# Kernel optimization log

Measured on AMD Instinct MI355X. Metric: run time of the kernel, lower is better.

## Reference

```python
import jax, jax.numpy as jnp
import numpy as np

N_NODES = 50000
N_EDGES = 800000
N_REL = 8
OUT_CH = 64      # latent dim of z
HID = 128        # hidden_channels
IN_CH = 128      # reconstructed feature dim
NEG_SLOPE = 0.2


def rgat_conv(x, src, dst, edge_type, weight, q, k, bias, num_nodes):
    """PyG RGATConv, heads=1, dim=1, additive-self-attention, across-relation.
    x: [N, in]; weight: [R, in, out]; q,k: [out, 1]; bias: [out]."""
    # per-relation transform of all nodes, then per-edge gather (same math as
    # per-edge bmm with weight[edge_type], avoids [E, in, out] intermediate)
    x_all = jnp.einsum('ni,rio->nro', x, weight)          # [N, R, out]
    x_j = x_all[src, edge_type]                            # [E, out]
    x_i = x_all[dst, edge_type]                            # [E, out]
    alpha = (x_i @ q + x_j @ k)[:, 0]                      # [E]
    alpha = jax.nn.leaky_relu(alpha, NEG_SLOPE)
    # scatter-softmax over destination neighborhoods
    m = jax.ops.segment_max(alpha, dst, num_segments=num_nodes)
    m = jnp.where(jnp.isfinite(m), m, 0.0)                 # empty segments -> 0
    ex = jnp.exp(alpha - m[dst])
    denom = jax.ops.segment_sum(ex, dst, num_segments=num_nodes)
    a = ex / (denom[dst] + 1e-16)                          # [E]
    out = jax.ops.segment_sum(a[:, None] * x_j, dst, num_segments=num_nodes)
    return out + bias


def setup_inputs() -> dict:
    key = jax.random.key(0)
    ks = jax.random.split(key, 12)
    z = jax.random.normal(ks[0], (N_NODES, OUT_CH), dtype=jnp.float32)
    edge_index = jax.random.randint(ks[1], (2, N_EDGES), 0, N_NODES, dtype=jnp.int32)
    edge_type = jax.random.randint(ks[2], (N_EDGES,), 0, N_REL, dtype=jnp.int32)

    def glorot(k_, shape):
        fan = shape[-2] + shape[-1]
        return jax.random.normal(k_, shape, dtype=jnp.float32) * jnp.sqrt(2.0 / fan)

    return {
        'z': z,
        'lin_w': glorot(ks[3], (HID, OUT_CH)),
        'lin_b': jnp.zeros((HID,), dtype=jnp.float32),
        'w1': glorot(ks[4], (N_REL, HID, HID)),
        'q1': glorot(ks[5], (HID, 1)),
        'k1': glorot(ks[6], (HID, 1)),
        'b1': jnp.zeros((HID,), dtype=jnp.float32),
        'w2': glorot(ks[7], (N_REL, HID, IN_CH)),
        'q2': glorot(ks[8], (IN_CH, 1)),
        'k2': glorot(ks[9], (IN_CH, 1)),
        'b2': jnp.zeros((IN_CH,), dtype=jnp.float32),
        'edge_index': edge_index,
        'edge_type': edge_type,
    }


def reference(z, lin_w, lin_b, w1, q1, k1, b1, w2, q2, k2, b2, edge_index, edge_type):
    num_nodes = z.shape[0]
    src, dst = edge_index[0], edge_index[1]
    h = z @ lin_w.T + lin_b                                 # nn.Linear
    h = jax.nn.relu(rgat_conv(h, src, dst, edge_type, w1, q1, k1, b1, num_nodes))
    # dropout is identity in eval mode
    recon_x = rgat_conv(h, src, dst, edge_type, w2, q2, k2, b2, num_nodes)
    return recon_x
```

## Files before the change

### kernel.cpp

```cpp
#include <hip/hip_runtime.h>
#include <hip/hip_bf16.h>
#include <cstdint>
#include <cstddef>

#define N_NODES 50000
#define N_EDGES 800000
#define NSEG    (N_NODES * 8)

using frag_t = __attribute__((ext_vector_type(8))) short;
using f32x4  = __attribute__((ext_vector_type(4))) float;

typedef const __attribute__((address_space(1))) void* gptr_t;
typedef __attribute__((address_space(3))) void* lptr_t;

__device__ __forceinline__ short f2bf(float x) {
    __hip_bfloat16 h = __float2bfloat16(x);
    return *reinterpret_cast<short*>(&h);
}
__device__ __forceinline__ float bf2f(unsigned int u) {
    union { unsigned int i; float f; } v;
    v.i = u << 16;
    return v.f;
}
__device__ __forceinline__ float bf2f_hi(unsigned int u) {
    union { unsigned int i; float f; } v;
    v.i = u & 0xFFFF0000u;
    return v.f;
}
__device__ __forceinline__ unsigned int packbf2(float lo, float hi) {
    unsigned int a = (unsigned short)f2bf(lo);
    unsigned int b = (unsigned short)f2bf(hi);
    return a | (b << 16);
}


__global__ void hist_kernel(const int* __restrict__ dst, const int* __restrict__ et,
                            int* __restrict__ deg8, int E) {
    int e = blockIdx.x * 256 + threadIdx.x;
    if (e < E) atomicAdd(&deg8[dst[e] * 8 + et[e]], 1);
}

__global__ __launch_bounds__(256) void scan_part(const int* __restrict__ deg8,
                                                 int* __restrict__ part, int M) {
    __shared__ int red[256];
    int t = threadIdx.x;
    int idx = blockIdx.x * 1024 + t * 4;
    int s = 0;
    if (idx + 3 < M) {
        int4 d = *(const int4*)(deg8 + idx);
        s = d.x + d.y + d.z + d.w;
    } else {
        for (int c = 0; c < 4; c++) if (idx + c < M) s += deg8[idx + c];
    }
    red[t] = s;
    __syncthreads();
    #pragma unroll
    for (int off = 128; off; off >>= 1) {
        if (t < off) red[t] += red[t + off];
        __syncthreads();
    }
    if (t == 0) part[blockIdx.x] = red[0];
}

__global__ __launch_bounds__(512) void scan_mid(int* __restrict__ part, int nparts,
                                                int* __restrict__ rowp, int M) {
    __shared__ int buf[512];
    int t = threadIdx.x;
    int own = (t < nparts) ? part[t] : 0;
    buf[t] = own;
    __syncthreads();
    for (int off = 1; off < 512; off <<= 1) {
        int v = buf[t];
        int u = (t >= off) ? buf[t - off] : 0;
        __syncthreads();
        buf[t] = v + u;
        __syncthreads();
    }
    if (t < nparts) part[t] = buf[t] - own;
    if (t == 511) rowp[M] = buf[511];
}

__global__ __launch_bounds__(256) void scan_fix(const int* __restrict__ deg8,
                                                const int* __restrict__ part,
                                                int* __restrict__ rowp,
                                                int* __restrict__ cursor, int M) {
    __shared__ int wsum[4];
    int t = threadIdx.x, lane = t & 63, w = t >> 6;
    int idx = blockIdx.x * 1024 + t * 4;
    int v0 = 0, v1 = 0, v2 = 0, v3 = 0;
    if (idx + 3 < M) {
        int4 d = *(const int4*)(deg8 + idx);
        v0 = d.x; v1 = d.y; v2 = d.z; v3 = d.w;
    } else {
        if (idx     < M) v0 = deg8[idx];
        if (idx + 1 < M) v1 = deg8[idx + 1];
        if (idx + 2 < M) v2 = deg8[idx + 2];
        if (idx + 3 < M) v3 = deg8[idx + 3];
    }
    int tsum = v0 + v1 + v2 + v3;
    int sc = tsum;
    #pragma unroll
    for (int off = 1; off < 64; off <<= 1) {
        int u = __shfl_up(sc, off, 64);
        if (lane >= off) sc += u;
    }
    if (lane == 63) wsum[w] = sc;
    __syncthreads();
    int woff = 0;
    for (int i = 0; i < w; i++) woff += wsum[i];
    int excl = part[blockIdx.x] + woff + sc - tsum;
    if (idx     < M) { rowp[idx]     = excl; cursor[idx]     = excl; } excl += v0;
    if (idx + 1 < M) { rowp[idx + 1] = excl; cursor[idx + 1] = excl; } excl += v1;
    if (idx + 2 < M) { rowp[idx + 2] = excl; cursor[idx + 2] = excl; } excl += v2;
    if (idx + 3 < M) { rowp[idx + 3] = excl; cursor[idx + 3] = excl; }
}

__global__ void fill_kernel(const int* __restrict__ src, const int* __restrict__ dst,
                            const int* __restrict__ et, int* __restrict__ cursor,
                            int* __restrict__ sorted, int E) {
    int e = blockIdx.x * 256 + threadIdx.x;
    if (e < E) {
        int pos = atomicAdd(&cursor[dst[e] * 8 + et[e]], 1);
        sorted[pos] = src[e] | (et[e] << 16);
    }
}


__global__ __launch_bounds__(256) void gemm_lin(const float* __restrict__ A,
                                                const float* __restrict__ B,
                                                const float* __restrict__ bias,
                                                unsigned short* __restrict__ hb, int N) {
    const int Kdim = 64;
    __shared__ float As[32][64];
    __shared__ float Bs[32][128];
    int t = threadIdx.x;
    int n0 = blockIdx.x * 64;
    int rg = t >> 4, cg = t & 15;
    int an = t >> 2, ak = (t & 3) * 8;
    float acc[4][8] = {};

    for (int k0 = 0; k0 < Kdim; k0 += 32) {
        int gn = n0 + an;
        if (gn < N) {
            const float* ap = A + (size_t)gn * Kdim + k0 + ak;
            float4 v0 = *(const float4*)ap;
            float4 v1 = *(const float4*)(ap + 4);
            As[ak + 0][an] = v0.x; As[ak + 1][an] = v0.y;
            As[ak + 2][an] = v0.z; As[ak + 3][an] = v0.w;
            As[ak + 4][an] = v1.x; As[ak + 5][an] = v1.y;
            As[ak + 6][an] = v1.z; As[ak + 7][an] = v1.w;
        } else {
            #pragma unroll
            for (int c = 0; c < 8; c++) As[ak + c][an] = 0.f;
        }
        {
            int o = t >> 1, kh = (t & 1) * 16;
            const float* bp = B + (size_t)o * Kdim + k0 + kh;
            #pragma unroll
            for (int j = 0; j < 4; j++) {
                float4 v = ((const float4*)bp)[j];
                Bs[kh + j * 4 + 0][o] = v.x;
                Bs[kh + j * 4 + 1][o] = v.y;
                Bs[kh + j * 4 + 2][o] = v.z;
                Bs[kh + j * 4 + 3][o] = v.w;
            }
        }
        __syncthreads();
        #pragma unroll
        for (int k = 0; k < 32; k++) {
            float a[4], b[8];
            *(float4*)&a[0] = *(const float4*)&As[k][rg * 4];
            *(float4*)&b[0] = *(const float4*)&Bs[k][cg * 8];
            *(float4*)&b[4] = *(const float4*)&Bs[k][cg * 8 + 4];
            #pragma unroll
            for (int i = 0; i < 4; i++)
                #pragma unroll
                for (int j = 0; j < 8; j++)
                    acc[i][j] = fmaf(a[i], b[j], acc[i][j]);
        }
        __syncthreads();
    }
    #pragma unroll
    for (int i = 0; i < 4; i++) {
        int gn = n0 + rg * 4 + i;
        if (gn < N) {
            unsigned short us[8];
            #pragma unroll
            for (int j = 0; j < 8; j++)
                us[j] = (unsigned short)f2bf(acc[i][j] + bias[cg * 8 + j]);
            *(int4*)(hb + (size_t)gn * 128 + cg * 8) = *(int4*)&us[0];
        }
    }
}


__global__ void wprep2_kernel(const float* __restrict__ W1, const float* __restrict__ q1v,
                              const float* __restrict__ k1v,
                              const float* __restrict__ W2, const float* __restrict__ q2v,
                              const float* __restrict__ k2v,
                              short* __restrict__ Bf1, short* __restrict__ Bf2,
                              float* __restrict__ wq1, float* __restrict__ wk1,
                              float* __restrict__ wq2, float* __restrict__ wk2) {
    int g0 = blockIdx.x * 256 + threadIdx.x;
    int layer = (g0 >= 133120) ? 1 : 0;
    int g = g0 - layer * 133120;
    const float* W  = layer ? W2  : W1;
    const float* qv = layer ? q2v : q1v;
    const float* kv = layer ? k2v : k1v;
    short* Bf = layer ? Bf2 : Bf1;
    float* wq = layer ? wq2 : wq1;
    float* wk = layer ? wk2 : wk1;

    if (g < 131072) {
        int kk = g >> 7, o = g & 127;
        float v = W[(size_t)kk * 128 + o];
        Bf[(((size_t)(kk >> 3) * 128) + o) * 8 + (kk & 7)] = f2bf(v);
        return;
    }
    int h = g - 131072;
    if (h < 2048) {
        int which = h >> 10;
        int r = (h >> 7) & 7;
        int i = h & 127;
        const float* vec = which ? kv : qv;
        const float* wrow = W + ((size_t)r * 128 + i) * 128;
        float acc = 0.f;
        #pragma unroll 4
        for (int o = 0; o < 128; o++) acc = fmaf(wrow[o], vec[o], acc);
        (which ? wk : wq)[r * 128 + i] = acc;
    }
}


__global__ __launch_bounds__(256) void qk_table_kernel(const unsigned short* __restrict__ xb,
                                                       const float* __restrict__ wq,
                                                       const float* __restrict__ wk,
                                                       float* __restrict__ Q,
                                                       float* __restrict__ K, int N) {
    int n = blockIdx.x * 256 + threadIdx.x;
    if (n >= N) return;
    const uint2* row = (const uint2*)(xb + (size_t)n * 128);
    float aq[8] = {}, ak[8] = {};
    for (int i = 0; i < 32; i++) {
        uint2 d = row[i];
        float x0 = bf2f(d.x & 0xFFFFu);
        float x1 = bf2f(d.x >> 16);
        float x2 = bf2f(d.y & 0xFFFFu);
        float x3 = bf2f(d.y >> 16);
        int c = i * 4;
        #pragma unroll
        for (int r = 0; r < 8; r++) {
            const float* wqr = wq + r * 128 + c;
            const float* wkr = wk + r * 128 + c;
            aq[r] = fmaf(x0, wqr[0], fmaf(x1, wqr[1], fmaf(x2, wqr[2], fmaf(x3, wqr[3], aq[r]))));
            ak[r] = fmaf(x0, wkr[0], fmaf(x1, wkr[1], fmaf(x2, wkr[2], fmaf(x3, wkr[3], ak[r]))));
        }
    }
    float4* qp = (float4*)(Q + (size_t)n * 8);
    qp[0] = *(float4*)&aq[0];
    qp[1] = *(float4*)&aq[4];
    float4* kp = (float4*)(K + (size_t)n * 8);
    kp[0] = *(float4*)&ak[0];
    kp[1] = *(float4*)&ak[4];
}


__global__ __launch_bounds__(512, 8) void fused_agg_gemm(
        const unsigned short* __restrict__ hb,
        const float* __restrict__ Q,
        const float* __restrict__ Kt,
        const int* __restrict__ rowp8,
        const int* __restrict__ sorted,
        const short* __restrict__ Bf,
        const float* __restrict__ bias,
        float* __restrict__ Cout,
        unsigned short* __restrict__ hbout,
        int N, int relu) {
    __shared__ short s_tile[16 * 1024];
    __shared__ uint2 stash[8][64];
    __shared__ int wcnt;
    unsigned int* sdw = (unsigned int*)s_tile;
    const char* hbB = (const char*)hb;

    int t = threadIdx.x;
    int w = t >> 6, lane = t & 63;
    int lhi = lane >> 4, llo = lane & 15;
    unsigned int lv4 = (unsigned int)lane * 4u;
    int n0 = blockIdx.x * 16;

    if (t == 0) wcnt = 0;
    __syncthreads();

    for (;;) {
        int row;
        if (lane == 0) row = atomicAdd(&wcnt, 1);
        row = __shfl(row, 0, 64);
        if (row >= 16) break;
        int n = n0 + row;
        float2 acc = {0.f, 0.f};
        int rcur = 0;
        auto flushw = [&](unsigned int val) {
            int kb = rcur * 16 + (lane >> 2);
            sdw[kb * 64 + ((row ^ (kb & 15)) * 4) + (lane & 3)] = val;
        };
        if (n >= N) {
            while (rcur < 8) { flushw(0u); rcur++; }
            continue;
        }
        int beg = rowp8[n * 8];
        int end = rowp8[n * 8 + 8];
        int deg = end - beg;
        if (deg == 0) {
            while (rcur < 8) { flushw(0u); rcur++; }
            continue;
        }

        if (deg <= 64) {
            int pk = 0;
            float a = -INFINITY;
            if (lane < deg) {
                pk = sorted[beg + lane];
                int srcn = pk & 0xFFFF, etj = pk >> 16;
                a = Q[(size_t)n * 8 + etj] + Kt[(size_t)srcn * 8 + etj];
                a = (a > 0.f) ? a : 0.2f * a;
            }
            float m = a;
            #pragma unroll
            for (int off = 32; off; off >>= 1) m = fmaxf(m, __shfl_xor(m, off, 64));
            float e = (lane < deg) ? __expf(a - m) : 0.f;
            float sum = e;
            #pragma unroll
            for (int off = 32; off; off >>= 1) sum += __shfl_xor(sum, off, 64);
            float wgt = e / (sum + 1e-16f);
            stash[w][lane] = make_uint2((unsigned int)(pk & 0xFFFF) << 8,
                                        (__float_as_uint(wgt) & ~7u) | (unsigned int)(pk >> 16));

            int j = 0;
            for (; j + 8 <= deg; j += 8) {
                uint2 ee[8]; unsigned int dd[8];
                #pragma unroll
                for (int i = 0; i < 8; i++) ee[i] = stash[w][j + i];
                #pragma unroll
                for (int i = 0; i < 8; i++)
                    dd[i] = *(const unsigned int*)(hbB + (ee[i].x | lv4));
                #pragma unroll
                for (int i = 0; i < 8; i++) {
                    int e0 = (int)(ee[i].y & 7u);
                    float w0 = __uint_as_float(ee[i].y);
                    while (rcur < e0) { flushw(packbf2(acc.x, acc.y)); acc.x = acc.y = 0.f; rcur++; }
                    acc.x = fmaf(w0, bf2f(dd[i]),    acc.x);
                    acc.y = fmaf(w0, bf2f_hi(dd[i]), acc.y);
                }
            }
            for (; j < deg; j++) {
                uint2 e1 = stash[w][j];
                unsigned int d0 = *(const unsigned int*)(hbB + (e1.x | lv4));
                int e0 = (int)(e1.y & 7u);
                float w0 = __uint_as_float(e1.y);
                while (rcur < e0) { flushw(packbf2(acc.x, acc.y)); acc.x = acc.y = 0.f; rcur++; }
                acc.x = fmaf(w0, bf2f(d0),    acc.x);
                acc.y = fmaf(w0, bf2f_hi(d0), acc.y);
            }
            while (rcur < 8) { flushw(packbf2(acc.x, acc.y)); acc.x = acc.y = 0.f; rcur++; }
        } else {
            auto logit = [&](int j) -> float {
                int pk2 = sorted[beg + j];
                int srcn = pk2 & 0xFFFF, etj = pk2 >> 16;
                float aa = Q[(size_t)n * 8 + etj] + Kt[(size_t)srcn * 8 + etj];
                return (aa > 0.f) ? aa : 0.2f * aa;
            };
            float m = -INFINITY;
            for (int j = lane; j < deg; j += 64) m = fmaxf(m, logit(j));
            #pragma unroll
            for (int off = 32; off; off >>= 1) m = fmaxf(m, __shfl_xor(m, off, 64));
            float sum = 0.f;
            for (int j = lane; j < deg; j += 64) sum += __expf(logit(j) - m);
            #pragma unroll
            for (int off = 32; off; off >>= 1) sum += __shfl_xor(sum, off, 64);
            float inv = 1.f / (sum + 1e-16f);

            for (int j0 = 0; j0 < deg; j0 += 64) {
                int cnt = min(64, deg - j0);
                if (lane < cnt) {
                    int pk = sorted[beg + j0 + lane];
                    int srcn = pk & 0xFFFF, etj = pk >> 16;
                    float aa = Q[(size_t)n * 8 + etj] + Kt[(size_t)srcn * 8 + etj];
                    aa = (aa > 0.f) ? aa : 0.2f * aa;
                    float wgt = __expf(aa - m) * inv;
                    stash[w][lane] = make_uint2((unsigned int)srcn << 8,
                                                (__float_as_uint(wgt) & ~7u) | (unsigned int)etj);
                }
                for (int j = 0; j < cnt; j++) {
                    uint2 e1 = stash[w][j];
                    unsigned int d0 = *(const unsigned int*)(hbB + (e1.x | lv4));
                    int e0 = (int)(e1.y & 7u);
                    float w0 = __uint_as_float(e1.y);
                    while (rcur < e0) { flushw(packbf2(acc.x, acc.y)); acc.x = acc.y = 0.f; rcur++; }
                    acc.x = fmaf(w0, bf2f(d0),    acc.x);
                    acc.y = fmaf(w0, bf2f_hi(d0), acc.y);
                }
            }
            while (rcur < 8) { flushw(packbf2(acc.x, acc.y)); acc.x = acc.y = 0.f; rcur++; }
        }
    }
    __syncthreads();

    int ctb = w;
    f32x4 acc0 = {};
    const char* BfB = (const char*)Bf;
    #pragma unroll 4
    for (int kq = 0; kq < 32; kq++) {
        int kb = kq * 4 + lhi;
        int d = kb * 64 + ((llo ^ (kb & 15)) * 4);
        frag_t a  = *(const frag_t*)(&sdw[d]);
        frag_t b0 = *(const frag_t*)(BfB + ((size_t)kb * 128 + ctb * 16 + llo) * 16);
        acc0 = __builtin_amdgcn_mfma_f32_16x16x32_bf16(a, b0, acc0, 0, 0, 0);
    }

    {
        int col = ctb * 16 + llo;
        float bv = bias[col];
        #pragma unroll
        for (int rg = 0; rg < 4; rg++) {
            int rown = n0 + lhi * 4 + rg;
            if (rown < N) {
                float v = acc0[rg] + bv;
                if (relu) v = fmaxf(v, 0.f);
                if (Cout)  Cout[(size_t)rown * 128 + col] = v;
                if (hbout) hbout[(size_t)rown * 128 + col] = (unsigned short)f2bf(v);
            }
        }
    }
}


extern "C" void kernel_launch(void* const* d_in, const int* in_sizes, int n_in,
                              void* d_out, int out_size, void* d_ws, size_t ws_size,
                              hipStream_t stream) {
    const float* z     = (const float*)d_in[0];
    const float* lin_w = (const float*)d_in[1];
    const float* lin_b = (const float*)d_in[2];
    const float* w1    = (const float*)d_in[3];
    const float* q1    = (const float*)d_in[4];
    const float* k1    = (const float*)d_in[5];
    const float* b1    = (const float*)d_in[6];
    const float* w2    = (const float*)d_in[7];
    const float* q2    = (const float*)d_in[8];
    const float* k2    = (const float*)d_in[9];
    const float* b2    = (const float*)d_in[10];
    const int*   ei    = (const int*)d_in[11];
    const int*   et    = (const int*)d_in[12];
    float* out = (float*)d_out;

    char* ws = (char*)d_ws;
    size_t off = 0;
    auto alloc = [&](size_t bytes) -> void* {
        void* p = ws + off;
        off += (bytes + 255) & ~(size_t)255;
        return p;
    };
    unsigned short* hb  = (unsigned short*)alloc((size_t)N_NODES * 128 * 2);
    unsigned short* hb2 = (unsigned short*)alloc((size_t)N_NODES * 128 * 2);
    float* Q     = (float*)alloc((size_t)N_NODES * 8 * 4);
    float* K     = (float*)alloc((size_t)N_NODES * 8 * 4);
    int* sorted  = (int*)alloc((size_t)N_EDGES * 4);
    int* deg8    = (int*)alloc((size_t)NSEG * 4);
    int* rowp8   = (int*)alloc((size_t)(NSEG + 1) * 4);
    int* cursor8 = (int*)alloc((size_t)NSEG * 4);
    int* part    = (int*)alloc(1024 * 4);
    float* wq1   = (float*)alloc(8 * 128 * 4);
    float* wk1   = (float*)alloc(8 * 128 * 4);
    float* wq2   = (float*)alloc(8 * 128 * 4);
    float* wk2   = (float*)alloc(8 * 128 * 4);
    short* Bf1   = (short*)alloc((size_t)1024 * 128 * 2);
    short* Bf2   = (short*)alloc((size_t)1024 * 128 * 2);

    const int* src = ei;
    const int* dst = ei + N_EDGES;

    const int M = NSEG;
    const int nparts = (M + 1023) / 1024;

    hipMemsetAsync(deg8, 0, (size_t)M * 4, stream);
    hist_kernel<<<(N_EDGES + 255) / 256, 256, 0, stream>>>(dst, et, deg8, N_EDGES);
    scan_part<<<nparts, 256, 0, stream>>>(deg8, part, M);
    scan_mid<<<1, 512, 0, stream>>>(part, nparts, rowp8, M);
    scan_fix<<<nparts, 256, 0, stream>>>(deg8, part, rowp8, cursor8, M);
    fill_kernel<<<(N_EDGES + 255) / 256, 256, 0, stream>>>(src, dst, et, cursor8, sorted, N_EDGES);

    gemm_lin<<<(N_NODES + 63) / 64, 256, 0, stream>>>(z, lin_w, lin_b, hb, N_NODES);

    wprep2_kernel<<<(2 * 133120 + 255) / 256, 256, 0, stream>>>(
        w1, q1, k1, w2, q2, k2, Bf1, Bf2, wq1, wk1, wq2, wk2);

    int fgrid = (N_NODES + 15) / 16;
    int qgrid = (N_NODES + 255) / 256;

    qk_table_kernel<<<qgrid, 256, 0, stream>>>(hb, wq1, wk1, Q, K, N_NODES);
    fused_agg_gemm<<<fgrid, 512, 0, stream>>>(hb, Q, K, rowp8, sorted, Bf1, b1,
                                              (float*)nullptr, hb2, N_NODES, 1);

    qk_table_kernel<<<qgrid, 256, 0, stream>>>(hb2, wq2, wk2, Q, K, N_NODES);
    fused_agg_gemm<<<fgrid, 512, 0, stream>>>(hb2, Q, K, rowp8, sorted, Bf2, b2,
                                              out, (unsigned short*)nullptr, N_NODES, 0);
}
```

Baseline: 370.3 us.

## Fuse per-node Q/K attention tables into the producing GEMM epilogues

Removes both standalone qk_table kernels. The linear-layer GEMM and the first aggregation+GEMM kernel now compute the next layer's per-relation Q/K projections in their epilogues, reading the freshly produced bf16 rows from shared memory. This avoids re-reading the hidden feature matrices from global memory and saves two launches. In exchange it adds extra barriers and epilogue work to the fused kernels, and it needs separate Q/K buffers for layer two so the second layer does not overwrite tables the first layer is still reading.

```diff
diff --git a/kernel.cpp b/kernel.cpp
--- a/kernel.cpp
+++ b/kernel.cpp
@@ -126,13 +126,18 @@
 }
 
 
-__global__ __launch_bounds__(256) void gemm_lin(const float* __restrict__ A,
-                                                const float* __restrict__ B,
-                                                const float* __restrict__ bias,
-                                                unsigned short* __restrict__ hb, int N) {
+__global__ __launch_bounds__(256) void gemm_lin_qk(const float* __restrict__ A,
+                                                   const float* __restrict__ B,
+                                                   const float* __restrict__ bias,
+                                                   const float* __restrict__ wq,
+                                                   const float* __restrict__ wk,
+                                                   unsigned short* __restrict__ hb,
+                                                   float* __restrict__ Q,
+                                                   float* __restrict__ Kt, int N) {
     const int Kdim = 64;
-    __shared__ float As[32][64];
-    __shared__ float Bs[32][128];
+    __shared__ float smem[32 * 64 + 32 * 128];
+    float (*As)[64]  = (float (*)[64])smem;
+    float (*Bs)[128] = (float (*)[128])(smem + 32 * 64);
     int t = threadIdx.x;
     int n0 = blockIdx.x * 64;
     int rg = t >> 4, cg = t & 15;
@@ -180,15 +185,54 @@
         }
         __syncthreads();
     }
+
+    unsigned short* hlds = (unsigned short*)smem;
     #pragma unroll
     for (int i = 0; i < 4; i++) {
         int gn = n0 + rg * 4 + i;
-        if (gn < N) {
-            unsigned short us[8];
-            #pragma unroll
-            for (int j = 0; j < 8; j++)
-                us[j] = (unsigned short)f2bf(acc[i][j] + bias[cg * 8 + j]);
+        unsigned short us[8];
+        #pragma unroll
+        for (int j = 0; j < 8; j++)
+            us[j] = (unsigned short)f2bf(acc[i][j] + bias[cg * 8 + j]);
+        if (gn < N)
             *(int4*)(hb + (size_t)gn * 128 + cg * 8) = *(int4*)&us[0];
+        *(int4*)(hlds + (size_t)(rg * 4 + i) * 128 + cg * 8) = *(int4*)&us[0];
+    }
+    __syncthreads();
+
+    {
+        int n = t >> 2, qq = t & 3;
+        int gn = n0 + n;
+        float aq[8] = {}, akk[8] = {};
+        const uint2* rowq = (const uint2*)(hlds + (size_t)n * 128 + qq * 32);
+        #pragma unroll
+        for (int i = 0; i < 8; i++) {
+            uint2 d = rowq[i];
+            float x0 = bf2f(d.x & 0xFFFFu);
+            float x1 = bf2f(d.x >> 16);
+            float x2 = bf2f(d.y & 0xFFFFu);
+            float x3 = bf2f(d.y >> 16);
+            int c = qq * 32 + i * 4;
+            #pragma unroll
+            for (int r = 0; r < 8; r++) {
+                const float* wqr = wq + r * 128 + c;
+                const float* wkr = wk + r * 128 + c;
+                aq[r]  = fmaf(x0, wqr[0], fmaf(x1, wqr[1], fmaf(x2, wqr[2], fmaf(x3, wqr[3], aq[r]))));
+                akk[r] = fmaf(x0, wkr[0], fmaf(x1, wkr[1], fmaf(x2, wkr[2], fmaf(x3, wkr[3], akk[r]))));
+            }
+        }
+        #pragma unroll
+        for (int r = 0; r < 8; r++) {
+            aq[r]  += __shfl_xor(aq[r], 1, 64);  aq[r]  += __shfl_xor(aq[r], 2, 64);
+            akk[r] += __shfl_xor(akk[r], 1, 64); akk[r] += __shfl_xor(akk[r], 2, 64);
+        }
+        if (qq == 0 && gn < N) {
+            float4* qp = (float4*)(Q + (size_t)gn * 8);
+            qp[0] = *(float4*)&aq[0];
+            qp[1] = *(float4*)&aq[4];
+            float4* kp = (float4*)(Kt + (size_t)gn * 8);
+            kp[0] = *(float4*)&akk[0];
+            kp[1] = *(float4*)&akk[4];
         }
     }
 }
@@ -232,39 +276,6 @@
 }
 
 
-__global__ __launch_bounds__(256) void qk_table_kernel(const unsigned short* __restrict__ xb,
-                                                       const float* __restrict__ wq,
-                                                       const float* __restrict__ wk,
-                                                       float* __restrict__ Q,
-                                                       float* __restrict__ K, int N) {
-    int n = blockIdx.x * 256 + threadIdx.x;
-    if (n >= N) return;
-    const uint2* row = (const uint2*)(xb + (size_t)n * 128);
-    float aq[8] = {}, ak[8] = {};
-    for (int i = 0; i < 32; i++) {
-        uint2 d = row[i];
-        float x0 = bf2f(d.x & 0xFFFFu);
-        float x1 = bf2f(d.x >> 16);
-        float x2 = bf2f(d.y & 0xFFFFu);
-        float x3 = bf2f(d.y >> 16);
-        int c = i * 4;
-        #pragma unroll
-        for (int r = 0; r < 8; r++) {
-            const float* wqr = wq + r * 128 + c;
-            const float* wkr = wk + r * 128 + c;
-            aq[r] = fmaf(x0, wqr[0], fmaf(x1, wqr[1], fmaf(x2, wqr[2], fmaf(x3, wqr[3], aq[r]))));
-            ak[r] = fmaf(x0, wkr[0], fmaf(x1, wkr[1], fmaf(x2, wkr[2], fmaf(x3, wkr[3], ak[r]))));
-        }
-    }
-    float4* qp = (float4*)(Q + (size_t)n * 8);
-    qp[0] = *(float4*)&aq[0];
-    qp[1] = *(float4*)&aq[4];
-    float4* kp = (float4*)(K + (size_t)n * 8);
-    kp[0] = *(float4*)&ak[0];
-    kp[1] = *(float4*)&ak[4];
-}
-
-
 __global__ __launch_bounds__(512, 8) void fused_agg_gemm(
         const unsigned short* __restrict__ hb,
         const float* __restrict__ Q,
@@ -273,6 +284,10 @@
         const int* __restrict__ sorted,
         const short* __restrict__ Bf,
         const float* __restrict__ bias,
+        const float* __restrict__ wqn,
+        const float* __restrict__ wkn,
+        float* __restrict__ Qout,
+        float* __restrict__ Kout,
         float* __restrict__ Cout,
         unsigned short* __restrict__ hbout,
         int N, int relu) {
@@ -417,17 +432,50 @@
         acc0 = __builtin_amdgcn_mfma_f32_16x16x32_bf16(a, b0, acc0, 0, 0, 0);
     }
 
+    unsigned short us2[4];
+    int col = ctb * 16 + llo;
     {
-        int col = ctb * 16 + llo;
         float bv = bias[col];
         #pragma unroll
         for (int rg = 0; rg < 4; rg++) {
+            float v = acc0[rg] + bv;
+            if (relu) v = fmaxf(v, 0.f);
+            us2[rg] = (unsigned short)f2bf(v);
             int rown = n0 + lhi * 4 + rg;
             if (rown < N) {
-                float v = acc0[rg] + bv;
-                if (relu) v = fmaxf(v, 0.f);
                 if (Cout)  Cout[(size_t)rown * 128 + col] = v;
-                if (hbout) hbout[(size_t)rown * 128 + col] = (unsigned short)f2bf(v);
+                if (hbout) hbout[(size_t)rown * 128 + col] = us2[rg];
+            }
+        }
+    }
+
+    if (Qout) {
+        __syncthreads();
+        unsigned short* qlds = (unsigned short*)s_tile;
+        #pragma unroll
+        for (int rg = 0; rg < 4; rg++)
+            qlds[(size_t)(lhi * 4 + rg) * 128 + col] = us2[rg];
+        __syncthreads();
+        if (t < 256) {
+            int n = t >> 4;
+            int rr = (t >> 1) & 7;
+            int which = t & 1;
+            int gn = n0 + n;
+            if (gn < N) {
+                const float* wv = which ? wkn : wqn;
+                const uint2* rowq = (const uint2*)(qlds + (size_t)n * 128);
+                float acc = 0.f;
+                #pragma unroll 8
+                for (int i = 0; i < 32; i++) {
+                    uint2 d = rowq[i];
+                    float x0 = bf2f(d.x & 0xFFFFu);
+                    float x1 = bf2f(d.x >> 16);
+                    float x2 = bf2f(d.y & 0xFFFFu);
+                    float x3 = bf2f(d.y >> 16);
+                    const float* wv4 = wv + rr * 128 + i * 4;
+                    acc = fmaf(x0, wv4[0], fmaf(x1, wv4[1], fmaf(x2, wv4[2], fmaf(x3, wv4[3], acc))));
+                }
+                (which ? Kout : Qout)[(size_t)gn * 8 + rr] = acc;
             }
         }
     }
@@ -463,6 +511,8 @@
     unsigned short* hb2 = (unsigned short*)alloc((size_t)N_NODES * 128 * 2);
     float* Q     = (float*)alloc((size_t)N_NODES * 8 * 4);
     float* K     = (float*)alloc((size_t)N_NODES * 8 * 4);
+    float* Qb    = (float*)alloc((size_t)N_NODES * 8 * 4);
+    float* Kb    = (float*)alloc((size_t)N_NODES * 8 * 4);
     int* sorted  = (int*)alloc((size_t)N_EDGES * 4);
     int* deg8    = (int*)alloc((size_t)NSEG * 4);
     int* rowp8   = (int*)alloc((size_t)(NSEG + 1) * 4);
@@ -488,19 +538,20 @@
     scan_fix<<<nparts, 256, 0, stream>>>(deg8, part, rowp8, cursor8, M);
     fill_kernel<<<(N_EDGES + 255) / 256, 256, 0, stream>>>(src, dst, et, cursor8, sorted, N_EDGES);
 
-    gemm_lin<<<(N_NODES + 63) / 64, 256, 0, stream>>>(z, lin_w, lin_b, hb, N_NODES);
-
     wprep2_kernel<<<(2 * 133120 + 255) / 256, 256, 0, stream>>>(
         w1, q1, k1, w2, q2, k2, Bf1, Bf2, wq1, wk1, wq2, wk2);
 
+    gemm_lin_qk<<<(N_NODES + 63) / 64, 256, 0, stream>>>(z, lin_w, lin_b, wq1, wk1,
+                                                         hb, Q, K, N_NODES);
+
     int fgrid = (N_NODES + 15) / 16;
-    int qgrid = (N_NODES + 255) / 256;
-
-    qk_table_kernel<<<qgrid, 256, 0, stream>>>(hb, wq1, wk1, Q, K, N_NODES);
+
     fused_agg_gemm<<<fgrid, 512, 0, stream>>>(hb, Q, K, rowp8, sorted, Bf1, b1,
+                                              wq2, wk2, Qb, Kb,
                                               (float*)nullptr, hb2, N_NODES, 1);
 
-    qk_table_kernel<<<qgrid, 256, 0, stream>>>(hb2, wq2, wk2, Q, K, N_NODES);
-    fused_agg_gemm<<<fgrid, 512, 0, stream>>>(hb2, Q, K, rowp8, sorted, Bf2, b2,
+    fused_agg_gemm<<<fgrid, 512, 0, stream>>>(hb2, Qb, Kb, rowp8, sorted, Bf2, b2,
+                                              (const float*)nullptr, (const float*)nullptr,
+                                              (float*)nullptr, (float*)nullptr,
                                               out, (unsigned short*)nullptr, N_NODES, 0);
 }
```

After: 428.1 us. 1.16x slower.

## Merge independent prep kernels into block-partitioned mega-kernels to cut launches

Applied to the files above, without the earlier changes.

Combines the edge histogram, weight preparation and the input linear GEMM into one launch, with block ranges selecting each role. Also merges the CSR fill pass with the layer-1 Q/K table computation, since they do not depend on each other. The goal is fewer kernel launches and letting independent work overlap on the GPU. In exchange, all blocks now carry the GEMM's shared-memory footprint and register pressure, which may lower occupancy for the lightweight histogram blocks.

```diff
diff --git a/kernel.cpp b/kernel.cpp
--- a/kernel.cpp
+++ b/kernel.cpp
@@ -6,6 +6,10 @@
 #define N_NODES 50000
 #define N_EDGES 800000
 #define NSEG    (N_NODES * 8)
+#define HIST_BLKS 3125
+#define WPREP_BLKS 1040
+#define GLIN_BLKS 782
+#define QK_BLKS 196
 
 using frag_t = __attribute__((ext_vector_type(8))) short;
 using f32x4  = __attribute__((ext_vector_type(4))) float;
@@ -34,11 +38,125 @@
 }
 
 
-__global__ void hist_kernel(const int* __restrict__ dst, const int* __restrict__ et,
-                            int* __restrict__ deg8, int E) {
-    int e = blockIdx.x * 256 + threadIdx.x;
-    if (e < E) atomicAdd(&deg8[dst[e] * 8 + et[e]], 1);
-}
+__global__ __launch_bounds__(256) void prep_mega(
+        const int* __restrict__ dst, const int* __restrict__ et,
+        int* __restrict__ deg8,
+        const float* __restrict__ W1, const float* __restrict__ q1v,
+        const float* __restrict__ k1v,
+        const float* __restrict__ W2, const float* __restrict__ q2v,
+        const float* __restrict__ k2v,
+        short* __restrict__ Bf1, short* __restrict__ Bf2,
+        float* __restrict__ wq1, float* __restrict__ wk1,
+        float* __restrict__ wq2, float* __restrict__ wk2,
+        const float* __restrict__ z, const float* __restrict__ lin_w,
+        const float* __restrict__ lin_b,
+        unsigned short* __restrict__ hb) {
+    __shared__ float smem[32 * 64 + 32 * 128];
+    int b = blockIdx.x, t = threadIdx.x;
+
+    if (b < HIST_BLKS) {
+        int e = b * 256 + t;
+        if (e < N_EDGES) atomicAdd(&deg8[dst[e] * 8 + et[e]], 1);
+        return;
+    }
+    b -= HIST_BLKS;
+
+    if (b < WPREP_BLKS) {
+        int g0 = b * 256 + t;
+        int layer = (g0 >= 133120) ? 1 : 0;
+        int g = g0 - layer * 133120;
+        const float* W  = layer ? W2  : W1;
+        const float* qv = layer ? q2v : q1v;
+        const float* kv = layer ? k2v : k1v;
+        short* Bf = layer ? Bf2 : Bf1;
+        float* wq = layer ? wq2 : wq1;
+        float* wk = layer ? wk2 : wk1;
+        if (g < 131072) {
+            int kk = g >> 7, o = g & 127;
+            float v = W[(size_t)kk * 128 + o];
+            Bf[(((size_t)(kk >> 3) * 128) + o) * 8 + (kk & 7)] = f2bf(v);
+        } else {
+            int h = g - 131072;
+            if (h < 2048) {
+                int which = h >> 10;
+                int r = (h >> 7) & 7;
+                int i = h & 127;
+                const float* vec = which ? kv : qv;
+                const float* wrow = W + ((size_t)r * 128 + i) * 128;
+                float acc = 0.f;
+                #pragma unroll 4
+                for (int o = 0; o < 128; o++) acc = fmaf(wrow[o], vec[o], acc);
+                (which ? wk : wq)[r * 128 + i] = acc;
+            }
+        }
+        return;
+    }
+    b -= WPREP_BLKS;
+
+    {
+        float (*As)[64]  = (float (*)[64])smem;
+        float (*Bs)[128] = (float (*)[128])(smem + 32 * 64);
+        const int Kdim = 64;
+        int n0 = b * 64;
+        int rg = t >> 4, cg = t & 15;
+        int an = t >> 2, ak = (t & 3) * 8;
+        float acc[4][8] = {};
+
+        for (int k0 = 0; k0 < Kdim; k0 += 32) {
+            int gn = n0 + an;
+            if (gn < N_NODES) {
+                const float* ap = z + (size_t)gn * Kdim + k0 + ak;
+                float4 v0 = *(const float4*)ap;
+                float4 v1 = *(const float4*)(ap + 4);
+                As[ak + 0][an] = v0.x; As[ak + 1][an] = v0.y;
+                As[ak + 2][an] = v0.z; As[ak + 3][an] = v0.w;
+                As[ak + 4][an] = v1.x; As[ak + 5][an] = v1.y;
+                As[ak + 6][an] = v1.z; As[ak + 7][an] = v1.w;
+            } else {
+                #pragma unroll
+                for (int c = 0; c < 8; c++) As[ak + c][an] = 0.f;
+            }
+            {
+                int o = t >> 1, kh = (t & 1) * 16;
+                const float* bp = lin_w + (size_t)o * Kdim + k0 + kh;
+                #pragma unroll
+                for (int j = 0; j < 4; j++) {
+                    float4 v = ((const float4*)bp)[j];
+                    Bs[kh + j * 4 + 0][o] = v.x;
+                    Bs[kh + j * 4 + 1][o] = v.y;
+                    Bs[kh + j * 4 + 2][o] = v.z;
+                    Bs[kh + j * 4 + 3][o] = v.w;
+                }
+            }
+            __syncthreads();
+            #pragma unroll
+            for (int k = 0; k < 32; k++) {
+                float a[4], bb[8];
+                *(float4*)&a[0] = *(const float4*)&As[k][rg * 4];
+                *(float4*)&bb[0] = *(const float4*)&Bs[k][cg * 8];
+                *(float4*)&bb[4] = *(const float4*)&Bs[k][cg * 8 + 4];
+                #pragma unroll
+                for (int i = 0; i < 4; i++)
+                    #pragma unroll
+                    for (int j = 0; j < 8; j++)
+                        acc[i][j] = fmaf(a[i], bb[j], acc[i][j]);
+            }
+            __syncthreads();
+        }
+        #pragma unroll
+        for (int i = 0; i < 4; i++) {
+            int gn = n0 + rg * 4 + i;
+            if (gn < N_NODES) {
+                unsigned short us[8];
+                #pragma unroll
+                for (int j = 0; j < 8; j++)
+                    us[j] = (unsigned short)f2bf(acc[i][j] + lin_b[cg * 8 + j]);
+                *(int4*)(hb + (size_t)gn * 128 + cg * 8) = *(int4*)&us[0];
+            }
+        }
+    }
+}
+
 
 __global__ __launch_bounds__(256) void scan_part(const int* __restrict__ deg8,
                                                  int* __restrict__ part, int M) {
@@ -115,120 +233,51 @@
     if (idx + 3 < M) { rowp[idx + 3] = excl; cursor[idx + 3] = excl; }
 }
 
-__global__ void fill_kernel(const int* __restrict__ src, const int* __restrict__ dst,
-                            const int* __restrict__ et, int* __restrict__ cursor,
-                            int* __restrict__ sorted, int E) {
-    int e = blockIdx.x * 256 + threadIdx.x;
-    if (e < E) {
-        int pos = atomicAdd(&cursor[dst[e] * 8 + et[e]], 1);
-        sorted[pos] = src[e] | (et[e] << 16);
-    }
-}
-
-
-__global__ __launch_bounds__(256) void gemm_lin(const float* __restrict__ A,
-                                                const float* __restrict__ B,
-                                                const float* __restrict__ bias,
-                                                unsigned short* __restrict__ hb, int N) {
-    const int Kdim = 64;
-    __shared__ float As[32][64];
-    __shared__ float Bs[32][128];
-    int t = threadIdx.x;
-    int n0 = blockIdx.x * 64;
-    int rg = t >> 4, cg = t & 15;
-    int an = t >> 2, ak = (t & 3) * 8;
-    float acc[4][8] = {};
-
-    for (int k0 = 0; k0 < Kdim; k0 += 32) {
-        int gn = n0 + an;
-        if (gn < N) {
-            const float* ap = A + (size_t)gn * Kdim + k0 + ak;
-            float4 v0 = *(const float4*)ap;
-            float4 v1 = *(const float4*)(ap + 4);
-            As[ak + 0][an] = v0.x; As[ak + 1][an] = v0.y;
-            As[ak + 2][an] = v0.z; As[ak + 3][an] = v0.w;
-            As[ak + 4][an] = v1.x; As[ak + 5][an] = v1.y;
-            As[ak + 6][an] = v1.z; As[ak + 7][an] = v1.w;
-        } else {
-            #pragma unroll
-            for (int c = 0; c < 8; c++) As[ak + c][an] = 0.f;
-        }
-        {
-            int o = t >> 1, kh = (t & 1) * 16;
-            const float* bp = B + (size_t)o * Kdim + k0 + kh;
-            #pragma unroll
-            for (int j = 0; j < 4; j++) {
-                float4 v = ((const float4*)bp)[j];
-                Bs[kh + j * 4 + 0][o] = v.x;
-                Bs[kh + j * 4 + 1][o] = v.y;
-                Bs[kh + j * 4 + 2][o] = v.z;
-                Bs[kh + j * 4 + 3][o] = v.w;
-            }
-        }
-        __syncthreads();
+
+__global__ __launch_bounds__(256) void fill_qk(
+        const int* __restrict__ src, const int* __restrict__ dst,
+        const int* __restrict__ et, int* __restrict__ cursor,
+        int* __restrict__ sorted,
+        const unsigned short* __restrict__ xb,
+        const float* __restrict__ wq, const float* __restrict__ wk,
+        float* __restrict__ Q, float* __restrict__ K) {
+    int b = blockIdx.x, t = threadIdx.x;
+
+    if (b < HIST_BLKS) {
+        int e = b * 256 + t;
+        if (e < N_EDGES) {
+            int pos = atomicAdd(&cursor[dst[e] * 8 + et[e]], 1);
+            sorted[pos] = src[e] | (et[e] << 16);
+        }
+        return;
+    }
+    b -= HIST_BLKS;
+
+    int n = b * 256 + t;
+    if (n >= N_NODES) return;
+    const uint2* row = (const uint2*)(xb + (size_t)n * 128);
+    float aq[8] = {}, ak[8] = {};
+    for (int i = 0; i < 32; i++) {
+        uint2 d = row[i];
+        float x0 = bf2f(d.x & 0xFFFFu);
+        float x1 = bf2f(d.x >> 16);
+        float x2 = bf2f(d.y & 0xFFFFu);
+        float x3 = bf2f(d.y >> 16);
+        int c = i * 4;
         #pragma unroll
-        for (int k = 0; k < 32; k++) {
-            float a[4], b[8];
-            *(float4*)&a[0] = *(const float4*)&As[k][rg * 4];
-            *(float4*)&b[0] = *(const float4*)&Bs[k][cg * 8];
-            *(float4*)&b[4] = *(const float4*)&Bs[k][cg * 8 + 4];
-            #pragma unroll
-            for (int i = 0; i < 4; i++)
-                #pragma unroll
-                for (int j = 0; j < 8; j++)
-                    acc[i][j] = fmaf(a[i], b[j], acc[i][j]);
-        }
-        __syncthreads();
-    }
-    #pragma unroll
-    for (int i = 0; i < 4; i++) {
-        int gn = n0 + rg * 4 + i;
-        if (gn < N) {
-            unsigned short us[8];
-            #pragma unroll
-            for (int j = 0; j < 8; j++)
-                us[j] = (unsigned short)f2bf(acc[i][j] + bias[cg * 8 + j]);
-            *(int4*)(hb + (size_t)gn * 128 + cg * 8) = *(int4*)&us[0];
-        }
-    }
-}
-
-
-__global__ void wprep2_kernel(const float* __restrict__ W1, const float* __restrict__ q1v,
-                              const float* __restrict__ k1v,
-                              const float* __restrict__ W2, const float* __restrict__ q2v,
-                              const float* __restrict__ k2v,
-                              short* __restrict__ Bf1, short* __restrict__ Bf2,
-                              float* __restrict__ wq1, float* __restrict__ wk1,
-                              float* __restrict__ wq2, float* __restrict__ wk2) {
-    int g0 = blockIdx.x * 256 + threadIdx.x;
-    int layer = (g0 >= 133120) ? 1 : 0;
-    int g = g0 - layer * 133120;
-    const float* W  = layer ? W2  : W1;
-    const float* qv = layer ? q2v : q1v;
-    const float* kv = layer ? k2v : k1v;
-    short* Bf = layer ? Bf2 : Bf1;
-    float* wq = layer ? wq2 : wq1;
-    float* wk = layer ? wk2 : wk1;
-
-    if (g < 131072) {
-        int kk = g >> 7, o = g & 127;
-        float v = W[(size_t)kk * 128 + o];
-        Bf[(((size_t)(kk >> 3) * 128) + o) * 8 + (kk & 7)] = f2bf(v);
-        return;
-    }
-    int h = g - 131072;
-    if (h < 2048) {
-        int which = h >> 10;
-        int r = (h >> 7) & 7;
-        int i = h & 127;
-        const float* vec = which ? kv : qv;
-        const float* wrow = W + ((size_t)r * 128 + i) * 128;
-        float acc = 0.f;
-        #pragma unroll 4
-        for (int o = 0; o < 128; o++) acc = fmaf(wrow[o], vec[o], acc);
-        (which ? wk : wq)[r * 128 + i] = acc;
-    }
+        for (int r = 0; r < 8; r++) {
+            const float* wqr = wq + r * 128 + c;
+            const float* wkr = wk + r * 128 + c;
+            aq[r] = fmaf(x0, wqr[0], fmaf(x1, wqr[1], fmaf(x2, wqr[2], fmaf(x3, wqr[3], aq[r]))));
+            ak[r] = fmaf(x0, wkr[0], fmaf(x1, wkr[1], fmaf(x2, wkr[2], fmaf(x3, wkr[3], ak[r]))));
+        }
+    }
+    float4* qp = (float4*)(Q + (size_t)n * 8);
+    qp[0] = *(float4*)&aq[0];
+    qp[1] = *(float4*)&aq[4];
+    float4* kp = (float4*)(K + (size_t)n * 8);
+    kp[0] = *(float4*)&ak[0];
+    kp[1] = *(float4*)&ak[4];
 }
 
 
@@ -482,25 +531,27 @@
     const int nparts = (M + 1023) / 1024;
 
     hipMemsetAsync(deg8, 0, (size_t)M * 4, stream);
-    hist_kernel<<<(N_EDGES + 255) / 256, 256, 0, stream>>>(dst, et, deg8, N_EDGES);
+
+    prep_mega<<<HIST_BLKS + WPREP_BLKS + GLIN_BLKS, 256, 0, stream>>>(
+        dst, et, deg8,
+        w1, q1, k1, w2, q2, k2, Bf1, Bf2, wq1, wk1, wq2, wk2,
+        z, lin_w, lin_b, hb);
+
     scan_part<<<nparts, 256, 0, stream>>>(deg8, part, M);
     scan_mid<<<1, 512, 0, stream>>>(part, nparts, rowp8, M);
     scan_fix<<<nparts, 256, 0, stream>>>(deg8, part, rowp8, cursor8, M);
-    fill_kernel<<<(N_EDGES + 255) / 256, 256, 0, stream>>>(src, dst, et, cursor8, sorted, N_EDGES);
-
-    gemm_lin<<<(N_NODES + 63) / 64, 256, 0, stream>>>(z, lin_w, lin_b, hb, N_NODES);
-
-    wprep2_kernel<<<(2 * 133120 + 255) / 256, 256, 0, stream>>>(
-        w1, q1, k1, w2, q2, k2, Bf1, Bf2, wq1, wk1, wq2, wk2);
+
+    fill_qk<<<HIST_BLKS + QK_BLKS, 256, 0, stream>>>(
+        src, dst, et, cursor8, sorted, hb, wq1, wk1, Q, K);
 
     int fgrid = (N_NODES + 15) / 16;
     int qgrid = (N_NODES + 255) / 256;
 
-    qk_table_kernel<<<qgrid, 256, 0, stream>>>(hb, wq1, wk1, Q, K, N_NODES);
     fused_agg_gemm<<<fgrid, 512, 0, stream>>>(hb, Q, K, rowp8, sorted, Bf1, b1,
                                               (float*)nullptr, hb2, N_NODES, 1);
 
     qk_table_kernel<<<qgrid, 256, 0, stream>>>(hb2, wq2, wk2, Q, K, N_NODES);
+
     fused_agg_gemm<<<fgrid, 512, 0, stream>>>(hb2, Q, K, rowp8, sorted, Bf2, b2,
                                               out, (unsigned short*)nullptr, N_NODES, 0);
 }
```

Result: faster. 349.0 us (-5.7%).
